# Kernel tuning notes

Measured on AMD Instinct MI355X. Metric: run time of the kernel, lower is better.

## Reference

```python
import jax, jax.numpy as jnp
import numpy as np

B, S, H = 2, 1024, 1024
NH, NKV, DH = 16, 4, 64
I, E, TOPK = 4096, 8, 2
EPS = 1e-5
ROPE_THETA = 10000.0


def setup_inputs() -> dict:
    key = jax.random.key(0)
    ks = jax.random.split(key, 16)
    std = 0.02
    inp = {
        'hidden_states': jax.random.normal(ks[0], (B, S, H), jnp.float32),
        'attention_mask': jnp.ones((B, S), jnp.int32),
        'position_ids': jnp.broadcast_to(jnp.arange(S, dtype=jnp.int32), (B, S)),
        'q_w': jax.random.normal(ks[1], (H, NH * DH), jnp.float32) * std,
        'k_w': jax.random.normal(ks[2], (H, NKV * DH), jnp.float32) * std,
        'v_w': jax.random.normal(ks[3], (H, NKV * DH), jnp.float32) * std,
        'o_w': jax.random.normal(ks[4], (NH * DH, H), jnp.float32) * std,
        'pre_attn_scale': jnp.ones((H,), jnp.float32),
        'post_attn_scale': jnp.ones((H,), jnp.float32),
        'pre_moe_scale': jnp.ones((H,), jnp.float32),
        'post_moe_scale': jnp.ones((H,), jnp.float32),
        'gate_w': jax.random.normal(ks[5], (H, E), jnp.float32) * std,
        'w_in': jax.random.normal(ks[6], (E, H, I), jnp.float32) * std,
        'w_v': jax.random.normal(ks[7], (E, H, I), jnp.float32) * std,
        'w_out': jax.random.normal(ks[8], (E, I, H), jnp.float32) * std,
    }
    return inp


def _rmsnorm(x, scale):
    var = jnp.mean(jnp.square(x), axis=-1, keepdims=True)
    return x * jax.lax.rsqrt(var + EPS) * scale


def _rope(x, positions):
    # x: [B, S, nheads, DH]; rotate-half RoPE
    half = DH // 2
    inv_freq = 1.0 / (ROPE_THETA ** (jnp.arange(0, half, dtype=jnp.float32) / half))
    ang = positions.astype(jnp.float32)[..., None] * inv_freq  # [B,S,half]
    cos = jnp.cos(ang)[:, :, None, :]
    sin = jnp.sin(ang)[:, :, None, :]
    x1, x2 = x[..., :half], x[..., half:]
    return jnp.concatenate([x1 * cos - x2 * sin, x2 * cos + x1 * sin], axis=-1)


def _attention(x, attention_mask, position_ids, q_w, k_w, v_w, o_w):
    q = (x @ q_w).reshape(B, S, NH, DH)
    k = (x @ k_w).reshape(B, S, NKV, DH)
    v = (x @ v_w).reshape(B, S, NKV, DH)
    q = _rope(q, position_ids)
    k = _rope(k, position_ids)
    groups = NH // NKV
    k = jnp.repeat(k, groups, axis=2)  # [B,S,NH,DH]
    v = jnp.repeat(v, groups, axis=2)
    scale = DH ** -0.5
    scores = jnp.einsum('bqhd,bkhd->bhqk', q, k) * scale
    causal = jnp.tril(jnp.ones((S, S), bool))
    valid = causal[None, None] & (attention_mask[:, None, None, :] > 0)
    scores = jnp.where(valid, scores, jnp.float32(-1e9))
    probs = jax.nn.softmax(scores, axis=-1)
    out = jnp.einsum('bhqk,bkhd->bqhd', probs, v).reshape(B, S, NH * DH)
    return out @ o_w


def _moe(x, gate_w, w_in, w_v, w_out):
    xf = x.reshape(-1, H)  # [T,H]
    T = xf.shape[0]
    logits = xf @ gate_w  # [T,E]
    probs = jax.nn.softmax(logits, axis=-1)
    top_w, top_i = jax.lax.top_k(probs, TOPK)  # Grok-1: no renormalization
    cw = jnp.zeros((T, E), xf.dtype).at[jnp.arange(T)[:, None], top_i].add(top_w)
    out = jnp.zeros_like(xf)
    for e in range(E):  # fixed small loop over experts
        h = jax.nn.gelu(xf @ w_in[e]) * (xf @ w_v[e])
        out = out + cw[:, e:e + 1] * (h @ w_out[e])
    return out.reshape(x.shape)


def reference(hidden_states, attention_mask, position_ids, q_w, k_w, v_w, o_w,
              pre_attn_scale, post_attn_scale, pre_moe_scale, post_moe_scale,
              gate_w, w_in, w_v, w_out):
    h = _rmsnorm(hidden_states, pre_attn_scale)
    attn = _attention(h, attention_mask, position_ids, q_w, k_w, v_w, o_w)
    attn = _rmsnorm(attn, post_attn_scale)
    x = hidden_states + attn
    h2 = _rmsnorm(x, pre_moe_scale)
    moe = _moe(h2, gate_w, w_in, w_v, w_out)
    moe = _rmsnorm(moe, post_moe_scale)
    return x + moe
```

## Files before the change

kernel.cpp:

```cpp
#include <hip/hip_runtime.h>
#include <hip/hip_bf16.h>
#include <math.h>

namespace {

constexpr int BB=2, SS=1024, HH=1024, NH=16, NKV=4, DH=64;
constexpr int II=4096, EE=8;
constexpr int TT=BB*SS;
constexpr int QKV=1536;
constexpr float EPS=1e-5f;

typedef __bf16 bf16x8 __attribute__((ext_vector_type(8)));
typedef float f32x4 __attribute__((ext_vector_type(4)));

__device__ __forceinline__ unsigned short f2bf(float x){
  union { float f; unsigned u; } un; un.f = x;
  unsigned r = un.u + 0x7fffu + ((un.u>>16)&1u);
  return (unsigned short)(r>>16);
}
__device__ __forceinline__ float bfval(unsigned short h){
  union { unsigned u; float f; } r; r.u = ((unsigned)h)<<16; return r.f;
}
__device__ __forceinline__ void split2(float v, unsigned short& hi, unsigned short& lo){
  hi = f2bf(v);
  lo = f2bf(v - bfval(hi));
}

__device__ __forceinline__ void gl_lds16(const void* g, void* l){
  __builtin_amdgcn_global_load_lds(
    (const __attribute__((address_space(1))) unsigned int*)g,
    (__attribute__((address_space(3))) unsigned int*)l, 16, 0, 0);
}

__device__ __forceinline__ float gelu_tanh(float x){
  float x3 = x*x*x;
  return 0.5f*x*(1.f + tanhf(0.7978845608028654f*(x + 0.044715f*x3)));
}

__global__ void rmsnorm_kernel(const float* __restrict__ in, const float* __restrict__ scale,
                               float* __restrict__ outf, unsigned short* __restrict__ outb,
                               unsigned short* __restrict__ outh, unsigned short* __restrict__ outl){
  int row = blockIdx.x, tid = threadIdx.x;
  const float* x = in + (size_t)row*HH;
  float ss = 0.f;
  for (int i=tid;i<HH;i+=256){ float v=x[i]; ss+=v*v; }
  __shared__ float red[256];
  red[tid]=ss; __syncthreads();
  for (int s=128;s>0;s>>=1){ if(tid<s) red[tid]+=red[tid+s]; __syncthreads(); }
  float inv = rsqrtf(red[0]/(float)HH + EPS);
  for (int i=tid;i<HH;i+=256){
    float v = x[i]*inv*scale[i];
    size_t o = (size_t)row*HH+i;
    if (outf) outf[o]=v;
    if (outb) outb[o]=f2bf(v);
    if (outh){ unsigned short h,l; split2(v,h,l); outh[o]=h; outl[o]=l; }
  }
}

__global__ void add_kernel(const float* __restrict__ a, const float* __restrict__ b,
                           float* __restrict__ o, int n){
  int i = blockIdx.x*256 + threadIdx.x;
  if (i < n) o[i] = a[i] + b[i];
}

__global__ void rope_split_kernel(const float* __restrict__ x, int stride, int off,
                                  const int* __restrict__ pos_ids,
                                  unsigned short* __restrict__ oh, unsigned short* __restrict__ ol,
                                  int nheads){
  int idx = blockIdx.x*256 + threadIdx.x;
  int total = TT*nheads*32;
  if (idx >= total) return;
  int j = idx & 31;
  int hh = (idx>>5) % nheads;
  int t = idx / (32*nheads);
  float pos = (float)pos_ids[t];
  float inv_freq = powf(10000.f, -(float)j/32.f);
  float ang = pos * inv_freq;
  float s, c; sincosf(ang, &s, &c);
  const float* p = x + (size_t)t*stride + off + hh*DH;
  float x1 = p[j], x2 = p[j+32];
  float r1 = x1*c - x2*s;
  float r2 = x2*c + x1*s;
  size_t o = ((size_t)t*nheads + hh)*DH;
  unsigned short h1,l1,h2,l2;
  split2(r1,h1,l1); split2(r2,h2,l2);
  oh[o+j]=h1;    ol[o+j]=l1;
  oh[o+j+32]=h2; ol[o+j+32]=l2;
}

__global__ __launch_bounds__(256) void vt_split_kernel(const float* __restrict__ src, int stride, int off,
    unsigned short* __restrict__ vth, unsigned short* __restrict__ vtl){
  int k0 = blockIdx.x*64;
  int kvh = blockIdx.y;
  int b = blockIdx.z;
  __shared__ float tile[64][65];
  int t = threadIdx.x;
  int c4 = (t&15)*4, gg = t>>4;
#pragma unroll
  for (int r=0;r<4;r++){
    int kk = gg + r*16;
    float4 v = *reinterpret_cast<const float4*>(src + (size_t)(b*SS+k0+kk)*stride + off + kvh*DH + c4);
    tile[kk][c4]=v.x; tile[kk][c4+1]=v.y; tile[kk][c4+2]=v.z; tile[kk][c4+3]=v.w;
  }
  __syncthreads();
#pragma unroll
  for (int r=0;r<4;r++){
    int dd = gg + r*16;
    ushort4 h4, l4v;
    split2(tile[c4  ][dd], h4.x, l4v.x);
    split2(tile[c4+1][dd], h4.y, l4v.y);
    split2(tile[c4+2][dd], h4.z, l4v.z);
    split2(tile[c4+3][dd], h4.w, l4v.w);
    size_t o = ((size_t)(b*NKV+kvh)*DH + dd)*SS + k0 + c4;
    *reinterpret_cast<ushort4*>(vth+o)=h4;
    *reinterpret_cast<ushort4*>(vtl+o)=l4v;
  }
}

__global__ __launch_bounds__(256) void attn_mfma(
    const unsigned short* __restrict__ qh, const unsigned short* __restrict__ ql,
    const unsigned short* __restrict__ khp, const unsigned short* __restrict__ klp,
    const unsigned short* __restrict__ vth, const unsigned short* __restrict__ vtl,
    const int* __restrict__ amask,
    unsigned short* __restrict__ ctxh, unsigned short* __restrict__ ctxl)
{
  int qb = blockIdx.x, h = blockIdx.y, b = blockIdx.z;
  int kvh = h >> 2;
  int tid = threadIdx.x;
  int w = tid >> 6, lane = tid & 63;
  int g = lane >> 4, l15 = lane & 15;

  __shared__ __align__(16) unsigned short Klh[64*64];
  __shared__ __align__(16) unsigned short Kll[64*64];
  __shared__ __align__(16) unsigned short Vlh[64*64];
  __shared__ __align__(16) unsigned short Vll[64*64];
  __shared__ __align__(16) unsigned short Pst[4][2][16*72];

  int q0w = qb*64 + w*16;

  bf16x8 qfh[2], qfl[2];
  {
    size_t qrow = ((size_t)(b*SS + q0w + l15)*NH + h)*DH;
#pragma unroll
    for (int ks=0; ks<2; ks++){
      qfh[ks] = *reinterpret_cast<const bf16x8*>(qh + qrow + ks*32 + g*8);
      qfl[ks] = *reinterpret_cast<const bf16x8*>(ql + qrow + ks*32 + g*8);
    }
  }

  f32x4 acc[4];
  float m_run[4], l_run[4];
#pragma unroll
  for (int i=0;i<4;i++){ acc[i]=f32x4{0,0,0,0}; m_run[i]=-1e30f; l_run[i]=0.f; }

  int nkv = qb + 1;
  for (int kblk=0; kblk<nkv; kblk++){
    int k0 = kblk*64;
    __syncthreads();
#pragma unroll
    for (int shot=0; shot<2; shot++){
      int a = shot*256 + tid;
      int row = a>>3, seg = a&7;
      int ss8 = (seg ^ (row&7))*8;
      int lo = row*64 + seg*8;
      size_t kg = ((size_t)(b*SS + k0 + row)*NKV + kvh)*DH + ss8;
      size_t vg = ((size_t)(b*NKV + kvh)*DH + row)*SS + k0 + ss8;
      gl_lds16(khp + kg, Klh + lo);
      gl_lds16(klp + kg, Kll + lo);
      gl_lds16(vth + vg, Vlh + lo);
      gl_lds16(vtl + vg, Vll + lo);
    }
    __syncthreads();

    f32x4 sf[4];
#pragma unroll
    for (int nf=0;nf<4;nf++) sf[nf]=f32x4{0,0,0,0};
#pragma unroll
    for (int ks=0; ks<2; ks++){
#pragma unroll
      for (int nf=0; nf<4; nf++){
        int krow = nf*16 + l15;
        int off = krow*64 + (((ks*4+g) ^ (krow&7))*8);
        bf16x8 bh = *reinterpret_cast<const bf16x8*>(Klh + off);
        bf16x8 bl = *reinterpret_cast<const bf16x8*>(Kll + off);
        sf[nf] = __builtin_amdgcn_mfma_f32_16x16x32_bf16(qfh[ks], bh, sf[nf],0,0,0);
        sf[nf] = __builtin_amdgcn_mfma_f32_16x16x32_bf16(qfh[ks], bl, sf[nf],0,0,0);
        sf[nf] = __builtin_amdgcn_mfma_f32_16x16x32_bf16(qfl[ks], bh, sf[nf],0,0,0);
      }
    }

    int am4[4];
#pragma unroll
    for (int nf=0;nf<4;nf++) am4[nf] = amask[b*SS + k0 + nf*16 + l15];
#pragma unroll
    for (int nf=0;nf<4;nf++){
      int k_abs = k0 + nf*16 + l15;
#pragma unroll
      for (int r=0;r<4;r++){
        float s = sf[nf][r]*0.125f;
        int q_abs = q0w + g*4 + r;
        if (k_abs > q_abs || am4[nf] <= 0) s = -1e9f;
        sf[nf][r] = s;
      }
    }

    float m_new[4], fsc[4];
#pragma unroll
    for (int r=0;r<4;r++){
      float v = fmaxf(fmaxf(sf[0][r],sf[1][r]), fmaxf(sf[2][r],sf[3][r]));
#pragma unroll
      for (int o=1;o<16;o<<=1) v = fmaxf(v, __shfl_xor(v,o));
      m_new[r] = fmaxf(m_run[r], v);
      fsc[r] = expf(m_run[r] - m_new[r]);
      m_run[r] = m_new[r];
    }

    unsigned short* Ph  = Pst[w][0];
    unsigned short* Plo = Pst[w][1];
    float rsum[4] = {0.f,0.f,0.f,0.f};
#pragma unroll
    for (int nf=0;nf<4;nf++){
#pragma unroll
      for (int r=0;r<4;r++){
        float p = expf(sf[nf][r] - m_new[r]);
        rsum[r] += p;
        unsigned short hi = f2bf(p);
        float lo = p - bfval(hi);
        Ph [(g*4+r)*72 + nf*16 + l15] = hi;
        Plo[(g*4+r)*72 + nf*16 + l15] = f2bf(lo);
      }
    }
#pragma unroll
    for (int r=0;r<4;r++){
#pragma unroll
      for (int o=1;o<16;o<<=1) rsum[r] += __shfl_xor(rsum[r],o);
      l_run[r] = l_run[r]*fsc[r] + rsum[r];
#pragma unroll
      for (int nf=0;nf<4;nf++) acc[nf][r] *= fsc[r];
    }

#pragma unroll
    for (int ks=0; ks<2; ks++){
      bf16x8 pa = *reinterpret_cast<const bf16x8*>(Ph  + l15*72 + ks*32 + g*8);
      bf16x8 pl = *reinterpret_cast<const bf16x8*>(Plo + l15*72 + ks*32 + g*8);
#pragma unroll
      for (int nf=0; nf<4; nf++){
        int drow = nf*16 + l15;
        int off = drow*64 + (((ks*4+g) ^ (drow&7))*8);
        bf16x8 vh = *reinterpret_cast<const bf16x8*>(Vlh + off);
        bf16x8 vl = *reinterpret_cast<const bf16x8*>(Vll + off);
        acc[nf] = __builtin_amdgcn_mfma_f32_16x16x32_bf16(pa, vh, acc[nf],0,0,0);
        acc[nf] = __builtin_amdgcn_mfma_f32_16x16x32_bf16(pa, vl, acc[nf],0,0,0);
        acc[nf] = __builtin_amdgcn_mfma_f32_16x16x32_bf16(pl, vh, acc[nf],0,0,0);
      }
    }
  }

#pragma unroll
  for (int r=0;r<4;r++){
    float inv = 1.f / l_run[r];
    size_t orow = ((size_t)(b*SS + q0w + g*4 + r)*NH + h)*DH;
#pragma unroll
    for (int nf=0;nf<4;nf++){
      float v = acc[nf][r]*inv;
      unsigned short hi,lo; split2(v,hi,lo);
      ctxh[orow + nf*16 + l15] = hi;
      ctxl[orow + nf*16 + l15] = lo;
    }
  }
}

__global__ void route_kernel(const float* __restrict__ x, const float* __restrict__ gw,
                             int* __restrict__ counts, int* __restrict__ lists,
                             float* __restrict__ cw){
  int t = blockIdx.x;
  int lane = threadIdx.x;
  float acc[EE];
#pragma unroll
  for (int e=0;e<EE;e++) acc[e]=0.f;
  for (int hh=lane; hh<HH; hh+=64){
    float xv = x[(size_t)t*HH + hh];
#pragma unroll
    for (int e=0;e<EE;e++) acc[e] += xv*gw[hh*EE+e];
  }
#pragma unroll
  for (int e=0;e<EE;e++){
#pragma unroll
    for (int off=1; off<64; off<<=1) acc[e] += __shfl_xor(acc[e], off);
  }
  if (lane==0){
    float m = acc[0];
    for (int e=1;e<EE;e++) m = fmaxf(m, acc[e]);
    float p[EE], s=0.f;
    for (int e=0;e<EE;e++){ p[e]=expf(acc[e]-m); s+=p[e]; }
    float invs = 1.f/s;
    for (int e=0;e<EE;e++) p[e]*=invs;
    int i1=0;
    for (int e=1;e<EE;e++) if (p[e]>p[i1]) i1=e;
    int i2 = (i1==0)?1:0;
    for (int e=0;e<EE;e++) if (e!=i1 && p[e]>p[i2]) i2=e;
    int pos = atomicAdd(&counts[i1],1);
    lists[i1*TT+pos]=t; cw[i1*TT+pos]=p[i1];
    pos = atomicAdd(&counts[i2],1);
    lists[i2*TT+pos]=t; cw[i2*TT+pos]=p[i2];
  }
}

__global__ void prefix_kernel(const int* __restrict__ c, int* __restrict__ b,
                              const float* __restrict__ cw, float* __restrict__ cw_slot){
  int lane = threadIdx.x;
  __shared__ int sb[EE+1];
  if (lane==0){
    int s=0;
    for (int e=0;e<EE;e++){ sb[e]=s; b[e]=s; s+=c[e]; }
    sb[EE]=s; b[EE]=s;
  }
  __syncthreads();
  for (int e=0;e<EE;e++){
    int cnt=c[e], base=sb[e];
    for (int i=lane;i<cnt;i+=64) cw_slot[base+i]=cw[e*TT+i];
  }
}

__global__ void moe_combine(const unsigned short* __restrict__ t0,
                            const unsigned short* __restrict__ t1,
                            const float* __restrict__ cwslot,
                            const int* __restrict__ ntotp,
                            unsigned short* __restrict__ ehb){
  int row = blockIdx.x;
  if (row >= *ntotp) return;
  float c = cwslot[row];
  size_t base = (size_t)row*II;
  int tid = threadIdx.x;
  for (int c0 = tid*8; c0 < II; c0 += 256*8){
    ushort4 x0 = *reinterpret_cast<const ushort4*>(t0+base+c0);
    ushort4 x1 = *reinterpret_cast<const ushort4*>(t0+base+c0+4);
    ushort4 y0 = *reinterpret_cast<const ushort4*>(t1+base+c0);
    ushort4 y1 = *reinterpret_cast<const ushort4*>(t1+base+c0+4);
    ushort4 o0, o1;
    o0.x = f2bf(gelu_tanh(bfval(x0.x))*bfval(y0.x)*c);
    o0.y = f2bf(gelu_tanh(bfval(x0.y))*bfval(y0.y)*c);
    o0.z = f2bf(gelu_tanh(bfval(x0.z))*bfval(y0.z)*c);
    o0.w = f2bf(gelu_tanh(bfval(x0.w))*bfval(y0.w)*c);
    o1.x = f2bf(gelu_tanh(bfval(x1.x))*bfval(y1.x)*c);
    o1.y = f2bf(gelu_tanh(bfval(x1.y))*bfval(y1.y)*c);
    o1.z = f2bf(gelu_tanh(bfval(x1.z))*bfval(y1.z)*c);
    o1.w = f2bf(gelu_tanh(bfval(x1.w))*bfval(y1.w)*c);
    *reinterpret_cast<ushort4*>(ehb+base+c0)   = o0;
    *reinterpret_cast<ushort4*>(ehb+base+c0+4) = o1;
  }
}

__global__ __launch_bounds__(256) void transpose_cvt(const float* __restrict__ in,
    unsigned short* __restrict__ out, int K, int N, size_t in_zstride, size_t out_zstride){
  __shared__ float tile[64][65];
  int k0 = blockIdx.x*64, n0 = blockIdx.y*64;
  const float* inz = in + in_zstride*blockIdx.z;
  unsigned short* outz = out + out_zstride*blockIdx.z;
  int t = threadIdx.x;
  int c4 = (t&15)*4, g = t>>4;
#pragma unroll
  for (int r=0;r<4;r++){
    int kk = g + r*16;
    float4 v = *reinterpret_cast<const float4*>(inz + (size_t)(k0+kk)*N + n0 + c4);
    tile[kk][c4]=v.x; tile[kk][c4+1]=v.y; tile[kk][c4+2]=v.z; tile[kk][c4+3]=v.w;
  }
  __syncthreads();
#pragma unroll
  for (int r=0;r<4;r++){
    int nn = g + r*16;
    ushort4 o;
    o.x=f2bf(tile[c4][nn]);   o.y=f2bf(tile[c4+1][nn]);
    o.z=f2bf(tile[c4+2][nn]); o.w=f2bf(tile[c4+3][nn]);
    *reinterpret_cast<ushort4*>(outz + (size_t)(n0+nn)*K + k0 + c4) = o;
  }
}

__global__ __launch_bounds__(256) void transpose_cvt_split(const float* __restrict__ in,
    unsigned short* __restrict__ oh, unsigned short* __restrict__ ol, int K, int N){
  __shared__ float tile[64][65];
  int k0 = blockIdx.x*64, n0 = blockIdx.y*64;
  int t = threadIdx.x;
  int c4 = (t&15)*4, g = t>>4;
#pragma unroll
  for (int r=0;r<4;r++){
    int kk = g + r*16;
    float4 v = *reinterpret_cast<const float4*>(in + (size_t)(k0+kk)*N + n0 + c4);
    tile[kk][c4]=v.x; tile[kk][c4+1]=v.y; tile[kk][c4+2]=v.z; tile[kk][c4+3]=v.w;
  }
  __syncthreads();
#pragma unroll
  for (int r=0;r<4;r++){
    int nn = g + r*16;
    ushort4 h4, l4v;
    split2(tile[c4  ][nn], h4.x, l4v.x);
    split2(tile[c4+1][nn], h4.y, l4v.y);
    split2(tile[c4+2][nn], h4.z, l4v.z);
    split2(tile[c4+3][nn], h4.w, l4v.w);
    size_t o = (size_t)(n0+nn)*K + k0 + c4;
    *reinterpret_cast<ushort4*>(oh + o) = h4;
    *reinterpret_cast<ushort4*>(ol + o) = l4v;
  }
}

__global__ __launch_bounds__(256,2) void mgemm_split(
    const unsigned short* __restrict__ Ah, const unsigned short* __restrict__ Alo,
    const unsigned short* __restrict__ Bh, const unsigned short* __restrict__ Blo,
    float* __restrict__ Cf, int NY, int N, int K)
{
  int bid = blockIdx.x;
  int qq = bid >> 7, rr = bid & 127;
  int xti = rr >> 3, sbit = rr & 7;
  int g = qq*8 + sbit;
  if (g >= NY) return;
  int row0 = xti*128, col0 = g*128;
  __shared__ __align__(16) unsigned short lds[32768];

  int t = threadIdx.x;
  int lane = t&63, w = t>>6, wr = w>>1, wc = w&1;
  int sr = t>>2, seg = t&3;

  f32x4 acc[4][4];
#pragma unroll
  for (int m=0;m<4;m++)
#pragma unroll
    for (int n=0;n<4;n++) acc[m][n]=f32x4{0,0,0,0};

  int l15 = lane&15, l4 = lane>>4;

  auto stage = [&](int buf, int k0){
    unsigned short* Lb = lds + buf*16384;
#pragma unroll
    for (int i=0;i<2;i++){
      int ldso = (sr + i*64)*32 + seg*8;
      size_t ar = (size_t)(row0 + sr + i*64);
      size_t br = (size_t)(col0 + sr + i*64);
      gl_lds16(Ah  + ar*K + k0 + seg*8, Lb +         ldso);
      gl_lds16(Alo + ar*K + k0 + seg*8, Lb + 4096  + ldso);
      gl_lds16(Bh  + br*K + k0 + seg*8, Lb + 8192  + ldso);
      gl_lds16(Blo + br*K + k0 + seg*8, Lb + 12288 + ldso);
    }
  };

  stage(0, 0);
  __syncthreads();
  int cur = 0;
  int NIT = K/32;
  for (int it=0; it<NIT; it++){
    if (it+1 < NIT) stage(cur^1, (it+1)*32);
    const unsigned short* Lb = lds + cur*16384;
    const bf16x8* Aph = reinterpret_cast<const bf16x8*>(Lb +         (wr*64 + l15)*32 + l4*8);
    const bf16x8* Apl = reinterpret_cast<const bf16x8*>(Lb + 4096  + (wr*64 + l15)*32 + l4*8);
    const bf16x8* Bph = reinterpret_cast<const bf16x8*>(Lb + 8192  + (wc*64 + l15)*32 + l4*8);
    const bf16x8* Bpl = reinterpret_cast<const bf16x8*>(Lb + 12288 + (wc*64 + l15)*32 + l4*8);
    bf16x8 ah[4], al[4], bh[4], bl[4];
#pragma unroll
    for (int m=0;m<4;m++){ ah[m]=Aph[m*64]; al[m]=Apl[m*64]; }
#pragma unroll
    for (int n=0;n<4;n++){ bh[n]=Bph[n*64]; bl[n]=Bpl[n*64]; }
#pragma unroll
    for (int m=0;m<4;m++)
#pragma unroll
      for (int n=0;n<4;n++){
        acc[m][n] = __builtin_amdgcn_mfma_f32_16x16x32_bf16(ah[m], bh[n], acc[m][n], 0,0,0);
        acc[m][n] = __builtin_amdgcn_mfma_f32_16x16x32_bf16(ah[m], bl[n], acc[m][n], 0,0,0);
        acc[m][n] = __builtin_amdgcn_mfma_f32_16x16x32_bf16(al[m], bh[n], acc[m][n], 0,0,0);
      }
    __syncthreads();
    cur ^= 1;
  }

#pragma unroll
  for (int m=0;m<4;m++){
    int rb = wr*64 + m*16 + l4*4;
#pragma unroll
    for (int n=0;n<4;n++){
      int col = col0 + wc*64 + n*16 + l15;
#pragma unroll
      for (int r=0;r<4;r++){
        int row = row0 + rb + r;
        Cf[(size_t)row*N + col] = acc[m][n][r];
      }
    }
  }
}

template<int MODE>
__global__ __launch_bounds__(256,3) void mgemm(
    const unsigned short* __restrict__ A, const unsigned short* __restrict__ B0b,
    const unsigned short* __restrict__ B1b, size_t bstride,
    float* __restrict__ Cf, unsigned short* __restrict__ Cb0, unsigned short* __restrict__ Cb1,
    int N, int K,
    const int* __restrict__ listb,
    const int* __restrict__ countb, const int* __restrict__ basep)
{
  int bid = blockIdx.x;
  int qq = bid >> 7, rr = bid & 127;
  int xti = rr >> 3, sbit = rr & 7;
  int g = qq*8 + sbit;
  int y, e;
  if (MODE==1){ y = g & 63; e = g >> 6; }
  else        { y = g & 15; e = g >> 4; }

  int M = countb[e];
  int row0 = xti*128;
  if (row0 >= M) return;
  int which = 0, col0, kbase = 0, KL = K;
  const unsigned short* B;
  if (MODE==1){
    which = y & 1;
    col0 = (y >> 1)*128;
    B = (which ? B1b : B0b) + bstride*e;
  } else {
    col0 = (y & 7)*128;
    kbase = (y >> 3)*(K/2);
    KL = K/2;
    B = B0b + bstride*e;
  }
  int slot = basep ? basep[e] : 0;
  const int* rowlist = listb + e*TT;

  __shared__ __align__(16) unsigned short lds[3][2][4096];

  int t = threadIdx.x;
  int lane = t&63, w = t>>6, wr = w>>1, wc = w&1;
  int sr = t>>2, seg = t&3;

  size_t arow[2], brow[2];
#pragma unroll
  for (int i=0;i<2;i++){
    int r = row0 + sr + i*64;
    int rc = (r < M) ? r : (M-1);
    if (MODE==1) arow[i] = (size_t)rowlist[rc];
    else         arow[i] = (size_t)(slot + rc);
    brow[i] = (size_t)(col0 + sr + i*64);
  }

  f32x4 acc[4][4];
#pragma unroll
  for (int m=0;m<4;m++)
#pragma unroll
    for (int n=0;n<4;n++) acc[m][n]=f32x4{0,0,0,0};

  int l15 = lane&15, l4 = lane>>4;

  auto stage = [&](int buf, int k0){
#pragma unroll
    for (int i=0;i<2;i++){
      int ldso = (sr + i*64)*32 + seg*8;
      gl_lds16(A + arow[i]*K + kbase + k0 + seg*8, &lds[buf][0][0] + ldso);
      gl_lds16(B + brow[i]*K + kbase + k0 + seg*8, &lds[buf][1][0] + ldso);
    }
  };

  int NIT = KL/32;
  stage(0, 0);
  if (NIT > 1) stage(1, 32);

  for (int it=0; it<NIT; it++){
    if (it+1 < NIT) asm volatile("s_waitcnt vmcnt(4)" ::: "memory");
    else            asm volatile("s_waitcnt vmcnt(0)" ::: "memory");
    __builtin_amdgcn_s_barrier();
    if (it+2 < NIT) stage((it+2)%3, (it+2)*32);

    int cb = it%3;
    const unsigned short* La = &lds[cb][0][0];
    const unsigned short* Lb = &lds[cb][1][0];
    bf16x8 af[4], bf[4];
#pragma unroll
    for (int m=0;m<4;m++)
      af[m] = *reinterpret_cast<const bf16x8*>(La + (wr*64 + m*16 + l15)*32 + l4*8);
#pragma unroll
    for (int n=0;n<4;n++)
      bf[n] = *reinterpret_cast<const bf16x8*>(Lb + (wc*64 + n*16 + l15)*32 + l4*8);
#pragma unroll
    for (int m=0;m<4;m++)
#pragma unroll
      for (int n=0;n<4;n++)
        acc[m][n] = __builtin_amdgcn_mfma_f32_16x16x32_bf16(af[m], bf[n], acc[m][n], 0,0,0);
  }

  unsigned short* Cb = which ? Cb1 : Cb0;
#pragma unroll
  for (int m=0;m<4;m++){
    int rb = wr*64 + m*16 + l4*4;
#pragma unroll
    for (int n=0;n<4;n++){
      int col = col0 + wc*64 + n*16 + l15;
#pragma unroll
      for (int r=0;r<4;r++){
        int row = row0 + rb + r;
        if (row >= M) continue;
        float v = acc[m][n][r];
        if (MODE==1){
          Cb[(size_t)(slot+row)*N + col] = f2bf(v);
        } else {
          atomicAdd(&Cf[(size_t)rowlist[row]*N + col], v);
        }
      }
    }
  }
}

}

extern "C" void kernel_launch(void* const* d_in, const int* in_sizes, int n_in,
                              void* d_out, int out_size, void* d_ws, size_t ws_size,
                              hipStream_t stream) {
  const float* hidden = (const float*)d_in[0];
  const int*   mask   = (const int*)d_in[1];
  const int*   pos    = (const int*)d_in[2];
  const float* q_w    = (const float*)d_in[3];
  const float* k_w    = (const float*)d_in[4];
  const float* v_w    = (const float*)d_in[5];
  const float* o_w    = (const float*)d_in[6];
  const float* pre_attn_scale  = (const float*)d_in[7];
  const float* post_attn_scale = (const float*)d_in[8];
  const float* pre_moe_scale   = (const float*)d_in[9];
  const float* post_moe_scale  = (const float*)d_in[10];
  const float* gate_w = (const float*)d_in[11];
  const float* w_in   = (const float*)d_in[12];
  const float* w_v    = (const float*)d_in[13];
  const float* w_out  = (const float*)d_in[14];
  float* out = (float*)d_out;

  char* base = (char*)d_ws;
  auto carve = [&](size_t bytes)->char*{
    char* r = base; base += (bytes + 255) & ~(size_t)255; return r;
  };
  float* hn  = (float*)carve((size_t)TT*HH*4);
  unsigned short* hnb = (unsigned short*)carve((size_t)TT*HH*2);
  unsigned short* hnh = (unsigned short*)carve((size_t)TT*HH*2);
  unsigned short* hnl = (unsigned short*)carve((size_t)TT*HH*2);
  float* qkvb = (float*)carve((size_t)TT*QKV*4);
  unsigned short* qsh = (unsigned short*)carve((size_t)TT*NH*DH*2);
  unsigned short* qsl = (unsigned short*)carve((size_t)TT*NH*DH*2);
  unsigned short* ksh = (unsigned short*)carve((size_t)TT*NKV*DH*2);
  unsigned short* ksl = (unsigned short*)carve((size_t)TT*NKV*DH*2);
  unsigned short* vth = (unsigned short*)carve((size_t)TT*NKV*DH*2);
  unsigned short* vtl = (unsigned short*)carve((size_t)TT*NKV*DH*2);
  unsigned short* ctxh = (unsigned short*)carve((size_t)TT*NH*DH*2);
  unsigned short* ctxl = (unsigned short*)carve((size_t)TT*NH*DH*2);
  float* ao  = (float*)carve((size_t)TT*HH*4);
  float* xb  = (float*)carve((size_t)TT*HH*4);
  float* moe = (float*)carve((size_t)TT*HH*4);
  float* cw  = (float*)carve((size_t)EE*TT*4);
  float* cw_slot = (float*)carve((size_t)2*TT*4);
  int* counts = (int*)carve(64*4);
  int* bases  = (int*)carve(64*4);
  int* lists  = (int*)carve((size_t)EE*TT*4);
  unsigned short* qkvwTh = (unsigned short*)carve((size_t)QKV*HH*2);
  unsigned short* qkvwTl = (unsigned short*)carve((size_t)QKV*HH*2);
  unsigned short* owTh = (unsigned short*)carve((size_t)NH*DH*HH*2);
  unsigned short* owTl = (unsigned short*)carve((size_t)NH*DH*HH*2);
  unsigned short* ehb   = (unsigned short*)carve((size_t)2*TT*II*2);
  unsigned short* tmp0  = (unsigned short*)carve((size_t)2*TT*II*2);
  unsigned short* tmp1  = (unsigned short*)carve((size_t)2*TT*II*2);
  unsigned short* winT  = (unsigned short*)carve((size_t)EE*II*HH*2);
  unsigned short* wvT   = (unsigned short*)carve((size_t)EE*II*HH*2);
  unsigned short* woutT = (unsigned short*)carve((size_t)EE*HH*II*2);
  size_t estride = (size_t)II*HH;

  rmsnorm_kernel<<<TT,256,0,stream>>>(hidden, pre_attn_scale, nullptr, nullptr, hnh, hnl);
  transpose_cvt_split<<<dim3(16,16),256,0,stream>>>(q_w, qkvwTh, qkvwTl, HH, NH*DH);
  transpose_cvt_split<<<dim3(16,4), 256,0,stream>>>(k_w, qkvwTh + (size_t)1024*HH, qkvwTl + (size_t)1024*HH, HH, NKV*DH);
  transpose_cvt_split<<<dim3(16,4), 256,0,stream>>>(v_w, qkvwTh + (size_t)1280*HH, qkvwTl + (size_t)1280*HH, HH, NKV*DH);
  transpose_cvt_split<<<dim3(16,16),256,0,stream>>>(o_w, owTh, owTl, NH*DH, HH);

  mgemm_split<<<2*128,256,0,stream>>>(hnh, hnl, qkvwTh, qkvwTl, qkvb, QKV/128, QKV, HH);

  rope_split_kernel<<<(TT*NH*32+255)/256,256,0,stream>>>(qkvb, QKV, 0, pos, qsh, qsl, NH);
  rope_split_kernel<<<(TT*NKV*32+255)/256,256,0,stream>>>(qkvb, QKV, 1024, pos, ksh, ksl, NKV);
  vt_split_kernel<<<dim3(SS/64,NKV,BB),256,0,stream>>>(qkvb, QKV, 1280, vth, vtl);

  attn_mfma<<<dim3(SS/64,NH,BB),256,0,stream>>>(qsh, qsl, ksh, ksl, vth, vtl, mask, ctxh, ctxl);

  mgemm_split<<<128,256,0,stream>>>(ctxh, ctxl, owTh, owTl, ao, HH/128, HH, NH*DH);
  rmsnorm_kernel<<<TT,256,0,stream>>>(ao, post_attn_scale, ao, nullptr, nullptr, nullptr);
  add_kernel<<<(TT*HH)/256,256,0,stream>>>(hidden, ao, xb, TT*HH);

  rmsnorm_kernel<<<TT,256,0,stream>>>(xb, pre_moe_scale, hn, hnb, nullptr, nullptr);
  hipMemsetAsync(counts, 0, 64*sizeof(int), stream);
  hipMemsetAsync(moe, 0, (size_t)TT*HH*sizeof(float), stream);
  route_kernel<<<TT,64,0,stream>>>(hn, gate_w, counts, lists, cw);
  prefix_kernel<<<1,64,0,stream>>>(counts, bases, cw, cw_slot);

  transpose_cvt<<<dim3(16,64,EE),256,0,stream>>>(w_in, winT, HH, II, (size_t)HH*II, estride);
  transpose_cvt<<<dim3(16,64,EE),256,0,stream>>>(w_v,  wvT,  HH, II, (size_t)HH*II, estride);
  transpose_cvt<<<dim3(64,16,EE),256,0,stream>>>(w_out, woutT, II, HH, (size_t)II*HH, estride);

  mgemm<1><<<16*64*EE,256,0,stream>>>(hnb, winT, wvT, estride, nullptr, tmp0, tmp1,
      II, HH, lists, counts, bases);
  moe_combine<<<2*TT,256,0,stream>>>(tmp0, tmp1, cw_slot, bases+EE, ehb);
  mgemm<2><<<16*16*EE,256,0,stream>>>(ehb, woutT, nullptr, estride, moe, nullptr, nullptr,
      HH, II, lists, counts, bases);

  rmsnorm_kernel<<<TT,256,0,stream>>>(moe, post_moe_scale, moe, nullptr, nullptr, nullptr);
  add_kernel<<<(TT*HH)/256,256,0,stream>>>(xb, moe, out, TT*HH);
}
```

Baseline: 633.1 us.

## Fuse norm/residual epilogues and swizzle LDS layout in GEMM kernels

Replaces the chains of rmsnorm and add kernels after attention and after the MoE with two fused per-row kernels. Each keeps the row in registers, so several full-tensor round trips through global memory and some kernel launches go away. Separately, both MFMA GEMM kernels now XOR-swizzle the global source k-offset against the LDS read offset. This is meant to cut LDS bank conflicts on the bf16x8 fragment reads. The swizzle must match exactly between the staging writes and the fragment reads, or results will be wrong.

```diff
diff --git a/kernel.cpp b/kernel.cpp
--- a/kernel.cpp
+++ b/kernel.cpp
@@ -57,10 +57,67 @@
   }
 }
 
-__global__ void add_kernel(const float* __restrict__ a, const float* __restrict__ b,
-                           float* __restrict__ o, int n){
-  int i = blockIdx.x*256 + threadIdx.x;
-  if (i < n) o[i] = a[i] + b[i];
+__global__ void fuse_attn_post(const float* __restrict__ ao_raw, const float* __restrict__ hidden,
+                               const float* __restrict__ post_scale, const float* __restrict__ pre_scale,
+                               float* __restrict__ xb, float* __restrict__ hn,
+                               unsigned short* __restrict__ hnb){
+  int row = blockIdx.x, tid = threadIdx.x;
+  const float* a = ao_raw + (size_t)row*HH;
+  const float* h = hidden + (size_t)row*HH;
+  float av[4], hv[4];
+  float ss = 0.f;
+#pragma unroll
+  for (int i=0;i<4;i++){
+    int idx = tid + i*256;
+    av[i]=a[idx]; hv[i]=h[idx];
+    ss += av[i]*av[i];
+  }
+  __shared__ float red[256];
+  red[tid]=ss; __syncthreads();
+  for (int s=128;s>0;s>>=1){ if(tid<s) red[tid]+=red[tid+s]; __syncthreads(); }
+  float inv1 = rsqrtf(red[0]/(float)HH + EPS);
+  __syncthreads();
+  float xv[4]; float ss2=0.f;
+#pragma unroll
+  for (int i=0;i<4;i++){
+    int idx = tid + i*256;
+    xv[i] = hv[i] + av[i]*inv1*post_scale[idx];
+    ss2 += xv[i]*xv[i];
+  }
+  red[tid]=ss2; __syncthreads();
+  for (int s=128;s>0;s>>=1){ if(tid<s) red[tid]+=red[tid+s]; __syncthreads(); }
+  float inv2 = rsqrtf(red[0]/(float)HH + EPS);
+#pragma unroll
+  for (int i=0;i<4;i++){
+    int idx = tid + i*256;
+    size_t o = (size_t)row*HH + idx;
+    xb[o] = xv[i];
+    float v = xv[i]*inv2*pre_scale[idx];
+    hn[o] = v;
+    hnb[o] = f2bf(v);
+  }
+}
+
+__global__ void fuse_moe_post(const float* __restrict__ moe, const float* __restrict__ xb,
+                              const float* __restrict__ scale, float* __restrict__ out){
+  int row = blockIdx.x, tid = threadIdx.x;
+  const float* m = moe + (size_t)row*HH;
+  float mv[4]; float ss=0.f;
+#pragma unroll
+  for (int i=0;i<4;i++){
+    int idx = tid + i*256;
+    mv[i]=m[idx]; ss += mv[i]*mv[i];
+  }
+  __shared__ float red[256];
+  red[tid]=ss; __syncthreads();
+  for (int s=128;s>0;s>>=1){ if(tid<s) red[tid]+=red[tid+s]; __syncthreads(); }
+  float inv = rsqrtf(red[0]/(float)HH + EPS);
+#pragma unroll
+  for (int i=0;i<4;i++){
+    int idx = tid + i*256;
+    size_t o = (size_t)row*HH + idx;
+    out[o] = xb[o] + mv[i]*inv*scale[idx];
+  }
 }
 
 __global__ void rope_split_kernel(const float* __restrict__ x, int stride, int off,
@@ -419,6 +476,7 @@
   int t = threadIdx.x;
   int lane = t&63, w = t>>6, wr = w>>1, wc = w&1;
   int sr = t>>2, seg = t&3;
+  int swzs = (t>>3)&3;
 
   f32x4 acc[4][4];
 #pragma unroll
@@ -427,18 +485,20 @@
     for (int n=0;n<4;n++) acc[m][n]=f32x4{0,0,0,0};
 
   int l15 = lane&15, l4 = lane>>4;
+  int swzr = (l15>>1)&3;
 
   auto stage = [&](int buf, int k0){
     unsigned short* Lb = lds + buf*16384;
+    int ksw = (seg ^ swzs)*8;
 #pragma unroll
     for (int i=0;i<2;i++){
       int ldso = (sr + i*64)*32 + seg*8;
       size_t ar = (size_t)(row0 + sr + i*64);
       size_t br = (size_t)(col0 + sr + i*64);
-      gl_lds16(Ah  + ar*K + k0 + seg*8, Lb +         ldso);
-      gl_lds16(Alo + ar*K + k0 + seg*8, Lb + 4096  + ldso);
-      gl_lds16(Bh  + br*K + k0 + seg*8, Lb + 8192  + ldso);
-      gl_lds16(Blo + br*K + k0 + seg*8, Lb + 12288 + ldso);
+      gl_lds16(Ah  + ar*K + k0 + ksw, Lb +         ldso);
+      gl_lds16(Alo + ar*K + k0 + ksw, Lb + 4096  + ldso);
+      gl_lds16(Bh  + br*K + k0 + ksw, Lb + 8192  + ldso);
+      gl_lds16(Blo + br*K + k0 + ksw, Lb + 12288 + ldso);
     }
   };
 
@@ -446,18 +506,23 @@
   __syncthreads();
   int cur = 0;
   int NIT = K/32;
+  int cofs = (l4 ^ swzr)*8;
   for (int it=0; it<NIT; it++){
     if (it+1 < NIT) stage(cur^1, (it+1)*32);
     const unsigned short* Lb = lds + cur*16384;
-    const bf16x8* Aph = reinterpret_cast<const bf16x8*>(Lb +         (wr*64 + l15)*32 + l4*8);
-    const bf16x8* Apl = reinterpret_cast<const bf16x8*>(Lb + 4096  + (wr*64 + l15)*32 + l4*8);
-    const bf16x8* Bph = reinterpret_cast<const bf16x8*>(Lb + 8192  + (wc*64 + l15)*32 + l4*8);
-    const bf16x8* Bpl = reinterpret_cast<const bf16x8*>(Lb + 12288 + (wc*64 + l15)*32 + l4*8);
     bf16x8 ah[4], al[4], bh[4], bl[4];
 #pragma unroll
-    for (int m=0;m<4;m++){ ah[m]=Aph[m*64]; al[m]=Apl[m*64]; }
-#pragma unroll
-    for (int n=0;n<4;n++){ bh[n]=Bph[n*64]; bl[n]=Bpl[n*64]; }
+    for (int m=0;m<4;m++){
+      int ro = (wr*64 + m*16 + l15)*32 + cofs;
+      ah[m]=*reinterpret_cast<const bf16x8*>(Lb +        ro);
+      al[m]=*reinterpret_cast<const bf16x8*>(Lb + 4096 + ro);
+    }
+#pragma unroll
+    for (int n=0;n<4;n++){
+      int ro = (wc*64 + n*16 + l15)*32 + cofs;
+      bh[n]=*reinterpret_cast<const bf16x8*>(Lb + 8192  + ro);
+      bl[n]=*reinterpret_cast<const bf16x8*>(Lb + 12288 + ro);
+    }
 #pragma unroll
     for (int m=0;m<4;m++)
 #pragma unroll
@@ -525,6 +590,7 @@
   int t = threadIdx.x;
   int lane = t&63, w = t>>6, wr = w>>1, wc = w&1;
   int sr = t>>2, seg = t&3;
+  int swzs = (t>>3)&3;
 
   size_t arow[2], brow[2];
 #pragma unroll
@@ -543,13 +609,15 @@
     for (int n=0;n<4;n++) acc[m][n]=f32x4{0,0,0,0};
 
   int l15 = lane&15, l4 = lane>>4;
+  int cofs = (l4 ^ ((l15>>1)&3))*8;
 
   auto stage = [&](int buf, int k0){
+    int ksw = (seg ^ swzs)*8;
 #pragma unroll
     for (int i=0;i<2;i++){
       int ldso = (sr + i*64)*32 + seg*8;
-      gl_lds16(A + arow[i]*K + kbase + k0 + seg*8, &lds[buf][0][0] + ldso);
-      gl_lds16(B + brow[i]*K + kbase + k0 + seg*8, &lds[buf][1][0] + ldso);
+      gl_lds16(A + arow[i]*K + kbase + k0 + ksw, &lds[buf][0][0] + ldso);
+      gl_lds16(B + brow[i]*K + kbase + k0 + ksw, &lds[buf][1][0] + ldso);
     }
   };
 
@@ -569,10 +637,10 @@
     bf16x8 af[4], bf[4];
 #pragma unroll
     for (int m=0;m<4;m++)
-      af[m] = *reinterpret_cast<const bf16x8*>(La + (wr*64 + m*16 + l15)*32 + l4*8);
+      af[m] = *reinterpret_cast<const bf16x8*>(La + (wr*64 + m*16 + l15)*32 + cofs);
 #pragma unroll
     for (int n=0;n<4;n++)
-      bf[n] = *reinterpret_cast<const bf16x8*>(Lb + (wc*64 + n*16 + l15)*32 + l4*8);
+      bf[n] = *reinterpret_cast<const bf16x8*>(Lb + (wc*64 + n*16 + l15)*32 + cofs);
 #pragma unroll
     for (int m=0;m<4;m++)
 #pragma unroll
@@ -676,10 +744,8 @@
   attn_mfma<<<dim3(SS/64,NH,BB),256,0,stream>>>(qsh, qsl, ksh, ksl, vth, vtl, mask, ctxh, ctxl);
 
   mgemm_split<<<128,256,0,stream>>>(ctxh, ctxl, owTh, owTl, ao, HH/128, HH, NH*DH);
-  rmsnorm_kernel<<<TT,256,0,stream>>>(ao, post_attn_scale, ao, nullptr, nullptr, nullptr);
-  add_kernel<<<(TT*HH)/256,256,0,stream>>>(hidden, ao, xb, TT*HH);
-
-  rmsnorm_kernel<<<TT,256,0,stream>>>(xb, pre_moe_scale, hn, hnb, nullptr, nullptr);
+  fuse_attn_post<<<TT,256,0,stream>>>(ao, hidden, post_attn_scale, pre_moe_scale, xb, hn, hnb);
+
   hipMemsetAsync(counts, 0, 64*sizeof(int), stream);
   hipMemsetAsync(moe, 0, (size_t)TT*HH*sizeof(float), stream);
   route_kernel<<<TT,64,0,stream>>>(hn, gate_w, counts, lists, cw);
@@ -695,6 +761,5 @@
   mgemm<2><<<16*16*EE,256,0,stream>>>(ehb, woutT, nullptr, estride, moe, nullptr, nullptr,
       HH, II, lists, counts, bases);
 
-  rmsnorm_kernel<<<TT,256,0,stream>>>(moe, post_moe_scale, moe, nullptr, nullptr, nullptr);
-  add_kernel<<<(TT*HH)/256,256,0,stream>>>(xb, moe, out, TT*HH);
-}
+  fuse_moe_post<<<TT,256,0,stream>>>(moe, xb, post_moe_scale, out);
+}
```

Result: faster. 607.0 us (-4.1%).
